# Kernel optimization log

Measured on AMD Instinct MI355X. Metric: run time of the kernel, lower is better.

## Reference

```python
import jax, jax.numpy as jnp
import numpy as np

B, N, DIM = 16, 1024, 768
H, HD = 12, 64  # num_heads, head_dim


def rotate_half(x):
    x1, x2 = jnp.split(x, 2, axis=-1)
    return jnp.concatenate((-x2, x1), axis=-1)


def setup_inputs() -> dict:
    key = jax.random.key(0)
    k1, k2, k3, k4, k5 = jax.random.split(key, 5)
    x = jax.random.normal(k1, (B, N, DIM), dtype=jnp.float32)
    # precomputed 2D-RoPE angles for the 32x32 patch grid: (N, head_dim)
    sin = jax.random.uniform(k2, (N, HD), dtype=jnp.float32, minval=-1.0, maxval=1.0)
    cos = jax.random.uniform(k3, (N, HD), dtype=jnp.float32, minval=-1.0, maxval=1.0)
    # params: qkv (no bias), proj (with bias)
    W_qkv = jax.random.normal(k4, (DIM, 3 * H * HD), dtype=jnp.float32) / np.sqrt(DIM)
    W_proj = jax.random.normal(k5, (H * HD, DIM), dtype=jnp.float32) / np.sqrt(H * HD)
    b_proj = jnp.zeros((DIM,), dtype=jnp.float32)
    return {"x": x, "sin": sin, "cos": cos, "W_qkv": W_qkv, "W_proj": W_proj, "b_proj": b_proj}


def reference(x, sin, cos, W_qkv, W_proj, b_proj):
    b, n, _ = x.shape
    qkv = (x @ W_qkv).reshape(b, n, 3, H, HD)
    q, k, v = jnp.moveaxis(qkv, 2, 0)          # each (b, n, H, HD)
    q = jnp.swapaxes(q, 1, 2)                  # (b, H, n, HD)
    k = jnp.swapaxes(k, 1, 2)
    v = jnp.swapaxes(v, 1, 2)
    # RoPE (prefix_tokens=0: apply to all tokens); sin/cos broadcast (n,HD)->(1,1,n,HD)
    s = sin[None, None]
    c = cos[None, None]
    q = q * c + rotate_half(q) * s
    k = k * c + rotate_half(k) * s
    # scaled dot-product attention (non-causal, no mask, no dropout)
    scale = 1.0 / jnp.sqrt(jnp.asarray(HD, dtype=q.dtype))
    scores = jnp.einsum('bhqd,bhkd->bhqk', q, k) * scale
    attn = jax.nn.softmax(scores, axis=-1)
    out = jnp.einsum('bhqk,bhkd->bhqd', attn, v)
    out = jnp.swapaxes(out, 1, 2).reshape(b, n, H * HD)
    return out @ W_proj + b_proj
```

## Files before the change

kernel.cpp:

```cpp
#include <hip/hip_runtime.h>


typedef __attribute__((ext_vector_type(8))) _Float16 fp16x8;
typedef __attribute__((ext_vector_type(4))) _Float16 h4;
typedef __attribute__((ext_vector_type(4))) float f32x4;

#define MFMA16(a, b, c) __builtin_amdgcn_mfma_f32_16x16x32_f16(a, b, c, 0, 0, 0)

__device__ __forceinline__ float fexp2(float x) {
    float r;
    asm volatile("v_exp_f32 %0, %1\n\ts_nop 0" : "=v"(r) : "v"(x));
    return r;
}

__device__ __forceinline__ void gload16(const _Float16* g, _Float16* s) {
    __builtin_amdgcn_global_load_lds(
        (const __attribute__((address_space(1))) unsigned int*)g,
        (__attribute__((address_space(3))) unsigned int*)s, 16, 0, 0);
}

__global__ __launch_bounds__(256) void tofp16_kernel(const float* __restrict__ in,
                                                     _Float16* __restrict__ outp, int n4) {
    int i = blockIdx.x * 256 + threadIdx.x;
    if (i >= n4) return;
    float4 v = ((const float4*)in)[i];
    h4 o;
    o[0] = (_Float16)v.x;
    o[1] = (_Float16)v.y;
    o[2] = (_Float16)v.z;
    o[3] = (_Float16)v.w;
    *(h4*)(outp + (size_t)i * 4) = o;
}

__global__ __launch_bounds__(256) void ttrans_kernel(const float* __restrict__ W,
                                                     _Float16* __restrict__ outp,
                                                     int rows, int cols) {
    __shared__ float tile[32][33];
    const int c0 = blockIdx.x * 32, r0 = blockIdx.y * 32;
    const int t = threadIdx.x;
#pragma unroll
    for (int i = 0; i < 4; ++i) {
        int idx = t + i * 256;
        int r = idx >> 5, c = idx & 31;
        tile[r][c] = W[(size_t)(r0 + r) * cols + c0 + c];
    }
    __syncthreads();
#pragma unroll
    for (int i = 0; i < 4; ++i) {
        int idx = t + i * 256;
        int rp = idx >> 5, cp = idx & 31;
        outp[(size_t)(c0 + rp) * rows + r0 + cp] = (_Float16)tile[cp][rp];
    }
}

__device__ __forceinline__ void gemm_core8(
    const _Float16* __restrict__ Ag, const _Float16* __restrict__ Bg,
    _Float16* lds, int m0, int n0, f32x4 (&acc)[4][4]) {
    constexpr int BUF = 12288;
    constexpr int OB = 8192;
    const int t = threadIdx.x, l = t & 63, w = t >> 6;
    const int wr = w >> 1, wc = w & 1;
    const int hi = l >> 4, qL = l & 15;

    const int scol = ((t & 3) ^ ((t >> 3) & 3)) << 3;
    const int srow = t >> 2;

    int afo[4], bfo[4];
#pragma unroll
    for (int i = 0; i < 4; ++i) {
        int r = wr * 64 + i * 16 + qL;
        afo[i] = r * 32 + ((hi ^ ((r >> 1) & 3)) << 3);
        int c = wc * 64 + i * 16 + qL;
        bfo[i] = OB + c * 32 + ((hi ^ ((c >> 1) & 3)) << 3);
    }

    auto stageA = [&](int kt, int b) {
        _Float16* base = lds + b * BUF;
        const int k0 = kt * 32;
        gload16(Ag + (size_t)(m0 + srow) * 768 + k0 + scol,
                base + (w * 16) * 32);
        gload16(Ag + (size_t)(m0 + 128 + srow) * 768 + k0 + scol,
                base + (128 + w * 16) * 32);
    };
    auto stageB = [&](int kt, int b) {
        _Float16* base = lds + b * BUF;
        const int k0 = kt * 32;
        gload16(Bg + (size_t)(n0 + srow) * 768 + k0 + scol,
                base + OB + (w * 16) * 32);
    };

    stageA(0, 0);
    stageB(0, 0);
    stageA(1, 1);
    stageB(1, 1);
    asm volatile("s_waitcnt vmcnt(3)" ::: "memory");
    __builtin_amdgcn_s_barrier();

    for (int kt = 0; kt < 24; ++kt) {
        const int bn = (kt + 2) % 3;
        _Float16* bb = lds + (kt % 3) * BUF;

        if (kt < 22) stageA(kt + 2, bn);
        fp16x8 af[4], bf[4];
#pragma unroll
        for (int j = 0; j < 4; ++j) bf[j] = *(const fp16x8*)(bb + bfo[j]);
#pragma unroll
        for (int i = 0; i < 2; ++i) af[i] = *(const fp16x8*)(bb + afo[i]);
        __builtin_amdgcn_s_barrier();
        asm volatile("s_waitcnt lgkmcnt(0)" ::: "memory");
        __builtin_amdgcn_s_setprio(1);
#pragma unroll
        for (int i = 0; i < 2; ++i)
#pragma unroll
            for (int j = 0; j < 4; ++j) acc[i][j] = MFMA16(af[i], bf[j], acc[i][j]);
        __builtin_amdgcn_s_setprio(0);
        __builtin_amdgcn_s_barrier();

        if (kt < 22) stageB(kt + 2, bn);
#pragma unroll
        for (int i = 2; i < 4; ++i) af[i] = *(const fp16x8*)(bb + afo[i]);
        __builtin_amdgcn_s_barrier();
        asm volatile("s_waitcnt lgkmcnt(0)" ::: "memory");
        __builtin_amdgcn_s_setprio(1);
#pragma unroll
        for (int i = 2; i < 4; ++i)
#pragma unroll
            for (int j = 0; j < 4; ++j) acc[i][j] = MFMA16(af[i], bf[j], acc[i][j]);
        __builtin_amdgcn_s_setprio(0);

        if (kt < 22)
            asm volatile("s_waitcnt vmcnt(3)" ::: "memory");
        else
            asm volatile("s_waitcnt vmcnt(0)" ::: "memory");
        __builtin_amdgcn_s_barrier();
    }
}

__global__ __launch_bounds__(512, 4) void qkv_gemm(
    const _Float16* __restrict__ Ag, const _Float16* __restrict__ Bg,
    const float* __restrict__ sinp, const float* __restrict__ cosp,
    _Float16* __restrict__ Qf, _Float16* __restrict__ Kf,
    _Float16* __restrict__ Vt) {
    __shared__ _Float16 lds[3 * 12288];
    const int t = threadIdx.x, l = t & 63, w = t >> 6;
    const int wr = w >> 1, wc = w & 1;
    const int hi = l >> 4, qL = l & 15;

    const int bid = blockIdx.x;
    const int xcd = bid & 7, local = bid >> 3;
    const int m0 = (xcd * 8 + (local & 7)) * 256;
    const int n0 = (local >> 3) * 128;

    f32x4 acc[4][4];
#pragma unroll
    for (int i = 0; i < 4; ++i)
#pragma unroll
        for (int j = 0; j < 4; ++j) acc[i][j] = (f32x4){0.f, 0.f, 0.f, 0.f};

    gemm_core8(Ag, Bg, lds, m0, n0, acc);

    const int colbase = n0 + wc * 64;
    const int sector = colbase / 768;
    const int h = (colbase % 768) >> 6;
    const float SC = 0.18033688011f;

    if (sector == 2) {
#pragma unroll
        for (int ms = 0; ms < 4; ++ms) {
            int mbase = m0 + wr * 64 + ms * 16 + hi * 4;
            int b = mbase >> 10, nb = mbase & 1023;
            int bh = b * 12 + h;
#pragma unroll
            for (int ns = 0; ns < 4; ++ns) {
                int d = ns * 16 + qL;
                h4 pk;
#pragma unroll
                for (int reg = 0; reg < 4; ++reg) pk[reg] = (_Float16)acc[ms][ns][reg];
                *(h4*)(Vt + ((size_t)bh * 64 + d) * 1024 + nb) = pk;
            }
        }
    } else if (sector == 0) {
#pragma unroll
        for (int ms = 0; ms < 4; ++ms) {
#pragma unroll
            for (int reg = 0; reg < 4; ++reg) {
                int m = m0 + wr * 64 + ms * 16 + hi * 4 + reg;
                int b = m >> 10, n = m & 1023;
                size_t base = ((size_t)(b * 12 + h) * 1024 + n) * 64;
#pragma unroll
                for (int p = 0; p < 2; ++p) {
                    int d = p * 16 + qL;
                    float c1 = cosp[n * 64 + d], s1 = sinp[n * 64 + d];
                    float c2 = cosp[n * 64 + d + 32], s2 = sinp[n * 64 + d + 32];
                    float vlo = acc[ms][p][reg], vhi = acc[ms][p + 2][reg];
                    Qf[base + d] = (_Float16)((vlo * c1 - vhi * s1) * SC);
                    Qf[base + d + 32] = (_Float16)((vhi * c2 + vlo * s2) * SC);
                }
            }
        }
    } else {
#pragma unroll
        for (int ms = 0; ms < 4; ++ms) {
#pragma unroll
            for (int reg = 0; reg < 4; ++reg) {
                int m = m0 + wr * 64 + ms * 16 + hi * 4 + reg;
                int b = m >> 10, n = m & 1023;
                size_t base = ((size_t)(b * 12 + h) * 1024 + n) * 64;
#pragma unroll
                for (int p = 0; p < 2; ++p) {
                    int d = p * 16 + qL;
                    float c1 = cosp[n * 64 + d], s1 = sinp[n * 64 + d];
                    float c2 = cosp[n * 64 + d + 32], s2 = sinp[n * 64 + d + 32];
                    float vlo = acc[ms][p][reg], vhi = acc[ms][p + 2][reg];
                    Kf[base + d] = (_Float16)(vlo * c1 - vhi * s1);
                    Kf[base + d + 32] = (_Float16)(vhi * c2 + vlo * s2);
                }
            }
        }
    }
}

__global__ __launch_bounds__(512, 4) void proj_gemm(
    const _Float16* __restrict__ Ag, const _Float16* __restrict__ Bg,
    const float* __restrict__ bias, float* __restrict__ out) {
    __shared__ _Float16 lds[3 * 12288];
    const int t = threadIdx.x, l = t & 63, w = t >> 6;
    const int wr = w >> 1, wc = w & 1;
    const int hi = l >> 4, qL = l & 15;

    const int bid = blockIdx.x;
    const int xcd = bid & 7, local = bid >> 3;
    const int m0 = (xcd * 8 + (local & 7)) * 256;
    const int n0 = (local >> 3) * 128;

    f32x4 acc[4][4];
#pragma unroll
    for (int i = 0; i < 4; ++i)
#pragma unroll
        for (int j = 0; j < 4; ++j) acc[i][j] = (f32x4){0.f, 0.f, 0.f, 0.f};

    gemm_core8(Ag, Bg, lds, m0, n0, acc);

#pragma unroll
    for (int ms = 0; ms < 4; ++ms) {
#pragma unroll
        for (int ns = 0; ns < 4; ++ns) {
            int col = n0 + wc * 64 + ns * 16 + qL;
            float bv = bias[col];
#pragma unroll
            for (int reg = 0; reg < 4; ++reg) {
                int m = m0 + wr * 64 + ms * 16 + hi * 4 + reg;
                out[(size_t)m * 768 + col] = acc[ms][ns][reg] + bv;
            }
        }
    }
}

__global__ __launch_bounds__(256, 3) void attn_kernel(
    const _Float16* __restrict__ Qf, const _Float16* __restrict__ Kfg,
    const _Float16* __restrict__ Vtg, _Float16* __restrict__ aof) {
    __shared__ _Float16 khs[2][64][64];
    __shared__ _Float16 vts[2][64][64];
    __shared__ _Float16 pbuf[4][32][72];

    const int t = threadIdx.x, l = t & 63, w = t >> 6;
    const int flat = blockIdx.x;
    const int xcd = flat & 7, idx = flat >> 3;
    const int bh = xcd * 24 + (idx >> 3);
    const int n0 = (idx & 7) * 128;
    const int bq = bh / 12, hh = bh % 12;
    const size_t base = (size_t)bh << 16;
    const int hi = l >> 4, qL = l & 15;

    fp16x8 qf[2][2];
#pragma unroll
    for (int q2 = 0; q2 < 2; ++q2)
#pragma unroll
        for (int kk = 0; kk < 2; ++kk) {
            size_t off = base + (size_t)(n0 + w * 32 + q2 * 16 + qL) * 64 +
                         kk * 32 + (hi << 3);
            qf[q2][kk] = *(const fp16x8*)(Qf + off);
        }

    const int r0 = w * 16;
    const int srow = l >> 3;
    const int scol = ((l & 7) ^ srow) << 3;
    const _Float16* kf_src = Kfg + base + (size_t)(r0 + srow) * 64 + scol;
    const _Float16* vt_src = Vtg + base + (size_t)(r0 + srow) * 1024 + scol;

    int kfo[4][2];
#pragma unroll
    for (int c = 0; c < 4; ++c)
#pragma unroll
        for (int kk = 0; kk < 2; ++kk) {
            int row = c * 16 + qL;
            int col16 = (kk << 2) | hi;
            kfo[c][kk] = row * 64 + ((col16 ^ (row & 7)) << 3);
        }

    f32x4 ot[4][2];
    float l_part[2] = {0.f, 0.f};
#pragma unroll
    for (int q2 = 0; q2 < 2; ++q2)
#pragma unroll
        for (int dt = 0; dt < 4; ++dt) ot[dt][q2] = (f32x4){0.f, 0.f, 0.f, 0.f};

    auto stage = [&](int kt, int b) {
        const _Float16* ks = kf_src + (size_t)kt * 4096;
        gload16(ks, &khs[b][r0][0]);
        gload16(ks + 512, &khs[b][r0 + 8][0]);
        const _Float16* vs = vt_src + kt * 64;
        gload16(vs, &vts[b][r0][0]);
        gload16(vs + 8 * 1024, &vts[b][r0 + 8][0]);
    };

    stage(0, 0);
    __syncthreads();

    for (int kt = 0; kt < 16; ++kt) {
        const int cur = kt & 1;
        if (kt < 15) stage(kt + 1, cur ^ 1);

        const _Float16* kb = &khs[cur][0][0];
        const _Float16* vb = &vts[cur][0][0];

        f32x4 s[4][2];
#pragma unroll
        for (int c = 0; c < 4; ++c) {
            fp16x8 kf0 = *(const fp16x8*)(kb + kfo[c][0]);
            fp16x8 kf1 = *(const fp16x8*)(kb + kfo[c][1]);
#pragma unroll
            for (int q2 = 0; q2 < 2; ++q2) {
                f32x4 a = (f32x4){0.f, 0.f, 0.f, 0.f};
                a = MFMA16(kf0, qf[q2][0], a);
                a = MFMA16(kf1, qf[q2][1], a);
                s[c][q2] = a;
            }
        }

#pragma unroll
        for (int q2 = 0; q2 < 2; ++q2) {
            const int prow = q2 * 16 + qL;
            float lsum = 0.f;
#pragma unroll
            for (int c = 0; c < 4; ++c) {
                float p0 = fexp2(s[c][q2][0] - 4.0f);
                float p1 = fexp2(s[c][q2][1] - 4.0f);
                float p2 = fexp2(s[c][q2][2] - 4.0f);
                float p3 = fexp2(s[c][q2][3] - 4.0f);
                lsum += (p0 + p1) + (p2 + p3);
                h4 pk;
                pk[0] = (_Float16)p0;
                pk[1] = (_Float16)p1;
                pk[2] = (_Float16)p2;
                pk[3] = (_Float16)p3;
                *(h4*)&pbuf[w][prow][c * 16 + (hi << 2)] = pk;
            }
            l_part[q2] += lsum;
        }

        fp16x8 pf[2][2];
#pragma unroll
        for (int q2 = 0; q2 < 2; ++q2)
#pragma unroll
            for (int ss = 0; ss < 2; ++ss)
                pf[q2][ss] = *(const fp16x8*)&pbuf[w][q2 * 16 + qL][ss * 32 + (hi << 3)];

#pragma unroll
        for (int dt = 0; dt < 4; ++dt) {
            fp16x8 v0 = *(const fp16x8*)(vb + kfo[dt][0]);
            fp16x8 v1 = *(const fp16x8*)(vb + kfo[dt][1]);
#pragma unroll
            for (int q2 = 0; q2 < 2; ++q2) {
                ot[dt][q2] = MFMA16(v0, pf[q2][0], ot[dt][q2]);
                ot[dt][q2] = MFMA16(v1, pf[q2][1], ot[dt][q2]);
            }
        }

        __syncthreads();
    }

#pragma unroll
    for (int q2 = 0; q2 < 2; ++q2) {
        float ls = l_part[q2];
        ls += __shfl_xor(ls, 16);
        ls += __shfl_xor(ls, 32);
        float inv = 1.0f / ls;
        int n = n0 + w * 32 + q2 * 16 + qL;
        size_t rowoff = ((size_t)(bq * 1024 + n)) * 768 + hh * 64 + (hi << 2);
#pragma unroll
        for (int dt = 0; dt < 4; ++dt) {
            h4 r;
#pragma unroll
            for (int reg = 0; reg < 4; ++reg) r[reg] = (_Float16)(ot[dt][q2][reg] * inv);
            *(h4*)(aof + rowoff + dt * 16) = r;
        }
    }
}

extern "C" void kernel_launch(void* const* d_in, const int* in_sizes, int n_in,
                              void* d_out, int out_size, void* d_ws, size_t ws_size,
                              hipStream_t stream) {
    const float* x = (const float*)d_in[0];
    const float* sinp = (const float*)d_in[1];
    const float* cosp = (const float*)d_in[2];
    const float* Wqkv = (const float*)d_in[3];
    const float* Wproj = (const float*)d_in[4];
    const float* bproj = (const float*)d_in[5];
    float* out = (float*)d_out;

    char* ws = (char*)d_ws;
    _Float16* xf  = (_Float16*)(ws);
    _Float16* wqt = (_Float16*)(ws + 25165824);
    _Float16* wpt = (_Float16*)(ws + 28704768);
    _Float16* Qf  = (_Float16*)(ws + 29884416);
    _Float16* Kf  = (_Float16*)(ws + 55050240);
    _Float16* Vt  = (_Float16*)(ws + 80216064);
    _Float16* aof = xf;

    tofp16_kernel<<<12288, 256, 0, stream>>>(x, xf, 3145728);
    ttrans_kernel<<<dim3(72, 24), 256, 0, stream>>>(Wqkv, wqt, 768, 2304);
    ttrans_kernel<<<dim3(24, 24), 256, 0, stream>>>(Wproj, wpt, 768, 768);
    qkv_gemm<<<1152, 512, 0, stream>>>(xf, wqt, sinp, cosp, Qf, Kf, Vt);
    attn_kernel<<<1536, 256, 0, stream>>>(Qf, Kf, Vt, aof);
    proj_gemm<<<384, 512, 0, stream>>>(aof, wpt, bproj, out);
}
```

Measured before the change: 194.7 us.

## Shrink GEMM tiles to 128x128 with 256-thread blocks and precompute interleaved RoPE table

Both GEMMs change from 256x128 tiles with 512 threads to 128x128 tiles with 256 threads. This doubles the grid size and cuts LDS use per block, and the staging loads and vmcnt waits are adjusted to match. A small new kernel packs cos/sin pairs into a float4 table, so the RoPE epilogue does one vector load where it used to do four scalar loads. The cost is lower per-block data reuse: A is now reloaded for every N tile with more blocks. It also adds one extra kernel launch.

```diff
diff --git a/kernel.cpp b/kernel.cpp
--- a/kernel.cpp
+++ b/kernel.cpp
@@ -53,11 +53,24 @@
     }
 }
 
-__device__ __forceinline__ void gemm_core8(
+__global__ __launch_bounds__(256) void ropetab_kernel(const float* __restrict__ sinp,
+                                                      const float* __restrict__ cosp,
+                                                      float4* __restrict__ tab) {
+    int idx = blockIdx.x * 256 + threadIdx.x;
+    int n = idx >> 5, d = idx & 31;
+    float4 v;
+    v.x = cosp[n * 64 + d];
+    v.y = sinp[n * 64 + d];
+    v.z = cosp[n * 64 + d + 32];
+    v.w = sinp[n * 64 + d + 32];
+    tab[idx] = v;
+}
+
+__device__ __forceinline__ void gemm_core128(
     const _Float16* __restrict__ Ag, const _Float16* __restrict__ Bg,
     _Float16* lds, int m0, int n0, f32x4 (&acc)[4][4]) {
-    constexpr int BUF = 12288;
-    constexpr int OB = 8192;
+    constexpr int BUF = 8192;
+    constexpr int OB = 4096;
     const int t = threadIdx.x, l = t & 63, w = t >> 6;
     const int wr = w >> 1, wc = w & 1;
     const int hi = l >> 4, qL = l & 15;
@@ -77,23 +90,24 @@
     auto stageA = [&](int kt, int b) {
         _Float16* base = lds + b * BUF;
         const int k0 = kt * 32;
-        gload16(Ag + (size_t)(m0 + srow) * 768 + k0 + scol,
-                base + (w * 16) * 32);
-        gload16(Ag + (size_t)(m0 + 128 + srow) * 768 + k0 + scol,
-                base + (128 + w * 16) * 32);
+        gload16(Ag + (size_t)(m0 + srow) * 768 + k0 + scol, base + (w * 16) * 32);
+        gload16(Ag + (size_t)(m0 + 64 + srow) * 768 + k0 + scol,
+                base + (64 + w * 16) * 32);
     };
     auto stageB = [&](int kt, int b) {
         _Float16* base = lds + b * BUF;
         const int k0 = kt * 32;
         gload16(Bg + (size_t)(n0 + srow) * 768 + k0 + scol,
                 base + OB + (w * 16) * 32);
+        gload16(Bg + (size_t)(n0 + 64 + srow) * 768 + k0 + scol,
+                base + OB + (64 + w * 16) * 32);
     };
 
     stageA(0, 0);
     stageB(0, 0);
     stageA(1, 1);
     stageB(1, 1);
-    asm volatile("s_waitcnt vmcnt(3)" ::: "memory");
+    asm volatile("s_waitcnt vmcnt(4)" ::: "memory");
     __builtin_amdgcn_s_barrier();
 
     for (int kt = 0; kt < 24; ++kt) {
@@ -129,27 +143,26 @@
         __builtin_amdgcn_s_setprio(0);
 
         if (kt < 22)
-            asm volatile("s_waitcnt vmcnt(3)" ::: "memory");
+            asm volatile("s_waitcnt vmcnt(4)" ::: "memory");
         else
             asm volatile("s_waitcnt vmcnt(0)" ::: "memory");
         __builtin_amdgcn_s_barrier();
     }
 }
 
-__global__ __launch_bounds__(512, 4) void qkv_gemm(
+__global__ __launch_bounds__(256, 3) void qkv_gemm(
     const _Float16* __restrict__ Ag, const _Float16* __restrict__ Bg,
-    const float* __restrict__ sinp, const float* __restrict__ cosp,
-    _Float16* __restrict__ Qf, _Float16* __restrict__ Kf,
-    _Float16* __restrict__ Vt) {
-    __shared__ _Float16 lds[3 * 12288];
+    const float4* __restrict__ tab, _Float16* __restrict__ Qf,
+    _Float16* __restrict__ Kf, _Float16* __restrict__ Vt) {
+    __shared__ _Float16 lds[3 * 8192];
     const int t = threadIdx.x, l = t & 63, w = t >> 6;
     const int wr = w >> 1, wc = w & 1;
     const int hi = l >> 4, qL = l & 15;
 
     const int bid = blockIdx.x;
     const int xcd = bid & 7, local = bid >> 3;
-    const int m0 = (xcd * 8 + (local & 7)) * 256;
-    const int n0 = (local >> 3) * 128;
+    const int m0 = (xcd * 16 + (local & 15)) * 128;
+    const int n0 = (local >> 4) * 128;
 
     f32x4 acc[4][4];
 #pragma unroll
@@ -157,7 +170,7 @@
 #pragma unroll
         for (int j = 0; j < 4; ++j) acc[i][j] = (f32x4){0.f, 0.f, 0.f, 0.f};
 
-    gemm_core8(Ag, Bg, lds, m0, n0, acc);
+    gemm_core128(Ag, Bg, lds, m0, n0, acc);
 
     const int colbase = n0 + wc * 64;
     const int sector = colbase / 768;
@@ -190,11 +203,10 @@
 #pragma unroll
                 for (int p = 0; p < 2; ++p) {
                     int d = p * 16 + qL;
-                    float c1 = cosp[n * 64 + d], s1 = sinp[n * 64 + d];
-                    float c2 = cosp[n * 64 + d + 32], s2 = sinp[n * 64 + d + 32];
+                    float4 cs = tab[n * 32 + d];
                     float vlo = acc[ms][p][reg], vhi = acc[ms][p + 2][reg];
-                    Qf[base + d] = (_Float16)((vlo * c1 - vhi * s1) * SC);
-                    Qf[base + d + 32] = (_Float16)((vhi * c2 + vlo * s2) * SC);
+                    Qf[base + d] = (_Float16)((vlo * cs.x - vhi * cs.y) * SC);
+                    Qf[base + d + 32] = (_Float16)((vhi * cs.z + vlo * cs.w) * SC);
                 }
             }
         }
@@ -209,29 +221,28 @@
 #pragma unroll
                 for (int p = 0; p < 2; ++p) {
                     int d = p * 16 + qL;
-                    float c1 = cosp[n * 64 + d], s1 = sinp[n * 64 + d];
-                    float c2 = cosp[n * 64 + d + 32], s2 = sinp[n * 64 + d + 32];
+                    float4 cs = tab[n * 32 + d];
                     float vlo = acc[ms][p][reg], vhi = acc[ms][p + 2][reg];
-                    Kf[base + d] = (_Float16)(vlo * c1 - vhi * s1);
-                    Kf[base + d + 32] = (_Float16)(vhi * c2 + vlo * s2);
+                    Kf[base + d] = (_Float16)(vlo * cs.x - vhi * cs.y);
+                    Kf[base + d + 32] = (_Float16)(vhi * cs.z + vlo * cs.w);
                 }
             }
         }
     }
 }
 
-__global__ __launch_bounds__(512, 4) void proj_gemm(
+__global__ __launch_bounds__(256, 3) void proj_gemm(
     const _Float16* __restrict__ Ag, const _Float16* __restrict__ Bg,
     const float* __restrict__ bias, float* __restrict__ out) {
-    __shared__ _Float16 lds[3 * 12288];
+    __shared__ _Float16 lds[3 * 8192];
     const int t = threadIdx.x, l = t & 63, w = t >> 6;
     const int wr = w >> 1, wc = w & 1;
     const int hi = l >> 4, qL = l & 15;
 
     const int bid = blockIdx.x;
     const int xcd = bid & 7, local = bid >> 3;
-    const int m0 = (xcd * 8 + (local & 7)) * 256;
-    const int n0 = (local >> 3) * 128;
+    const int m0 = (xcd * 16 + (local & 15)) * 128;
+    const int n0 = (local >> 4) * 128;
 
     f32x4 acc[4][4];
 #pragma unroll
@@ -239,7 +250,7 @@
 #pragma unroll
         for (int j = 0; j < 4; ++j) acc[i][j] = (f32x4){0.f, 0.f, 0.f, 0.f};
 
-    gemm_core8(Ag, Bg, lds, m0, n0, acc);
+    gemm_core128(Ag, Bg, lds, m0, n0, acc);
 
 #pragma unroll
     for (int ms = 0; ms < 4; ++ms) {
@@ -416,12 +427,14 @@
     _Float16* Qf  = (_Float16*)(ws + 29884416);
     _Float16* Kf  = (_Float16*)(ws + 55050240);
     _Float16* Vt  = (_Float16*)(ws + 80216064);
+    float4*   tab = (float4*)(ws + 105381888);
     _Float16* aof = xf;
 
     tofp16_kernel<<<12288, 256, 0, stream>>>(x, xf, 3145728);
     ttrans_kernel<<<dim3(72, 24), 256, 0, stream>>>(Wqkv, wqt, 768, 2304);
     ttrans_kernel<<<dim3(24, 24), 256, 0, stream>>>(Wproj, wpt, 768, 768);
-    qkv_gemm<<<1152, 512, 0, stream>>>(xf, wqt, sinp, cosp, Qf, Kf, Vt);
+    ropetab_kernel<<<128, 256, 0, stream>>>(sinp, cosp, tab);
+    qkv_gemm<<<2304, 256, 0, stream>>>(xf, wqt, tab, Qf, Kf, Vt);
     attn_kernel<<<1536, 256, 0, stream>>>(Qf, Kf, Vt, aof);
-    proj_gemm<<<384, 512, 0, stream>>>(aof, wpt, bproj, out);
-}
+    proj_gemm<<<768, 256, 0, stream>>>(aof, wpt, bproj, out);
+}
```

After: 200.4 us. 3.0% more time.

## Swap MFMA operands for row-contiguous epilogue stores and split QKV GEMM

Applied to the files above, without the earlier changes.

For the Q/K and projection GEMMs, the MFMA operands are swapped so each lane's accumulator holds 4 consecutive columns of a single row. This lets the epilogues write packed h4 or float4 vectors instead of scattered scalar stores. A small kernel interleaves cos/sin into a float4 table so the RoPE epilogue loads one float4 per element instead of four scalars. The fused QKV GEMM is split into a Q/K launch and a separate V launch so each keeps its own store layout, at the cost of two extra kernel launches and a tail boundary between the GEMMs.

```diff
diff --git a/kernel.cpp b/kernel.cpp
--- a/kernel.cpp
+++ b/kernel.cpp
@@ -53,6 +53,20 @@
     }
 }
 
+__global__ __launch_bounds__(256) void ropetab_kernel(const float* __restrict__ sinp,
+                                                      const float* __restrict__ cosp,
+                                                      float4* __restrict__ tab) {
+    int idx = blockIdx.x * 256 + threadIdx.x;
+    int n = idx >> 5, d = idx & 31;
+    float4 v;
+    v.x = cosp[n * 64 + d];
+    v.y = sinp[n * 64 + d];
+    v.z = cosp[n * 64 + d + 32];
+    v.w = sinp[n * 64 + d + 32];
+    tab[idx] = v;
+}
+
+template <bool SWAP>
 __device__ __forceinline__ void gemm_core8(
     const _Float16* __restrict__ Ag, const _Float16* __restrict__ Bg,
     _Float16* lds, int m0, int n0, f32x4 (&acc)[4][4]) {
@@ -112,7 +126,12 @@
 #pragma unroll
         for (int i = 0; i < 2; ++i)
 #pragma unroll
-            for (int j = 0; j < 4; ++j) acc[i][j] = MFMA16(af[i], bf[j], acc[i][j]);
+            for (int j = 0; j < 4; ++j) {
+                if constexpr (SWAP)
+                    acc[i][j] = MFMA16(bf[j], af[i], acc[i][j]);
+                else
+                    acc[i][j] = MFMA16(af[i], bf[j], acc[i][j]);
+            }
         __builtin_amdgcn_s_setprio(0);
         __builtin_amdgcn_s_barrier();
 
@@ -125,7 +144,12 @@
 #pragma unroll
         for (int i = 2; i < 4; ++i)
 #pragma unroll
-            for (int j = 0; j < 4; ++j) acc[i][j] = MFMA16(af[i], bf[j], acc[i][j]);
+            for (int j = 0; j < 4; ++j) {
+                if constexpr (SWAP)
+                    acc[i][j] = MFMA16(bf[j], af[i], acc[i][j]);
+                else
+                    acc[i][j] = MFMA16(af[i], bf[j], acc[i][j]);
+            }
         __builtin_amdgcn_s_setprio(0);
 
         if (kt < 22)
@@ -136,10 +160,59 @@
     }
 }
 
-__global__ __launch_bounds__(512, 4) void qkv_gemm(
+__global__ __launch_bounds__(512, 4) void qkv_qk_gemm(
     const _Float16* __restrict__ Ag, const _Float16* __restrict__ Bg,
-    const float* __restrict__ sinp, const float* __restrict__ cosp,
-    _Float16* __restrict__ Qf, _Float16* __restrict__ Kf,
+    const float4* __restrict__ tab, _Float16* __restrict__ Qf,
+    _Float16* __restrict__ Kf) {
+    __shared__ _Float16 lds[3 * 12288];
+    const int t = threadIdx.x, l = t & 63, w = t >> 6;
+    const int wr = w >> 1, wc = w & 1;
+    const int hi = l >> 4, qL = l & 15;
+
+    const int bid = blockIdx.x;
+    const int xcd = bid & 7, local = bid >> 3;
+    const int m0 = (xcd * 8 + (local & 7)) * 256;
+    const int n0 = (local >> 3) * 128;
+
+    f32x4 acc[4][4];
+#pragma unroll
+    for (int i = 0; i < 4; ++i)
+#pragma unroll
+        for (int j = 0; j < 4; ++j) acc[i][j] = (f32x4){0.f, 0.f, 0.f, 0.f};
+
+    gemm_core8<true>(Ag, Bg, lds, m0, n0, acc);
+
+    const int colbase = n0 + wc * 64;
+    const int sector = colbase / 768;
+    const int h = (colbase % 768) >> 6;
+    _Float16* dst = (sector == 0) ? Qf : Kf;
+    const float SC = (sector == 0) ? 0.18033688011f : 1.0f;
+
+#pragma unroll
+    for (int ms = 0; ms < 4; ++ms) {
+        int m = m0 + wr * 64 + ms * 16 + qL;
+        int b = m >> 10, n = m & 1023;
+        size_t base = ((size_t)(b * 12 + h) * 1024 + n) * 64;
+#pragma unroll
+        for (int ns = 0; ns < 2; ++ns) {
+            int d0 = ns * 16 + hi * 4;
+            h4 lo4, hi4;
+#pragma unroll
+            for (int reg = 0; reg < 4; ++reg) {
+                int d = d0 + reg;
+                float4 cs = tab[n * 32 + d];
+                float vlo = acc[ms][ns][reg], vhi = acc[ms][ns + 2][reg];
+                lo4[reg] = (_Float16)((vlo * cs.x - vhi * cs.y) * SC);
+                hi4[reg] = (_Float16)((vhi * cs.z + vlo * cs.w) * SC);
+            }
+            *(h4*)(dst + base + d0) = lo4;
+            *(h4*)(dst + base + d0 + 32) = hi4;
+        }
+    }
+}
+
+__global__ __launch_bounds__(512, 4) void qkv_v_gemm(
+    const _Float16* __restrict__ Ag, const _Float16* __restrict__ Bg,
     _Float16* __restrict__ Vt) {
     __shared__ _Float16 lds[3 * 12288];
     const int t = threadIdx.x, l = t & 63, w = t >> 6;
@@ -149,7 +222,7 @@
     const int bid = blockIdx.x;
     const int xcd = bid & 7, local = bid >> 3;
     const int m0 = (xcd * 8 + (local & 7)) * 256;
-    const int n0 = (local >> 3) * 128;
+    const int n0 = (12 + (local >> 3)) * 128;
 
     f32x4 acc[4][4];
 #pragma unroll
@@ -157,65 +230,22 @@
 #pragma unroll
         for (int j = 0; j < 4; ++j) acc[i][j] = (f32x4){0.f, 0.f, 0.f, 0.f};
 
-    gemm_core8(Ag, Bg, lds, m0, n0, acc);
-
-    const int colbase = n0 + wc * 64;
-    const int sector = colbase / 768;
-    const int h = (colbase % 768) >> 6;
-    const float SC = 0.18033688011f;
-
-    if (sector == 2) {
-#pragma unroll
-        for (int ms = 0; ms < 4; ++ms) {
-            int mbase = m0 + wr * 64 + ms * 16 + hi * 4;
-            int b = mbase >> 10, nb = mbase & 1023;
-            int bh = b * 12 + h;
-#pragma unroll
-            for (int ns = 0; ns < 4; ++ns) {
-                int d = ns * 16 + qL;
-                h4 pk;
-#pragma unroll
-                for (int reg = 0; reg < 4; ++reg) pk[reg] = (_Float16)acc[ms][ns][reg];
-                *(h4*)(Vt + ((size_t)bh * 64 + d) * 1024 + nb) = pk;
-            }
-        }
-    } else if (sector == 0) {
-#pragma unroll
-        for (int ms = 0; ms < 4; ++ms) {
-#pragma unroll
-            for (int reg = 0; reg < 4; ++reg) {
-                int m = m0 + wr * 64 + ms * 16 + hi * 4 + reg;
-                int b = m >> 10, n = m & 1023;
-                size_t base = ((size_t)(b * 12 + h) * 1024 + n) * 64;
-#pragma unroll
-                for (int p = 0; p < 2; ++p) {
-                    int d = p * 16 + qL;
-                    float c1 = cosp[n * 64 + d], s1 = sinp[n * 64 + d];
-                    float c2 = cosp[n * 64 + d + 32], s2 = sinp[n * 64 + d + 32];
-                    float vlo = acc[ms][p][reg], vhi = acc[ms][p + 2][reg];
-                    Qf[base + d] = (_Float16)((vlo * c1 - vhi * s1) * SC);
-                    Qf[base + d + 32] = (_Float16)((vhi * c2 + vlo * s2) * SC);
-                }
-            }
-        }
-    } else {
-#pragma unroll
-        for (int ms = 0; ms < 4; ++ms) {
-#pragma unroll
-            for (int reg = 0; reg < 4; ++reg) {
-                int m = m0 + wr * 64 + ms * 16 + hi * 4 + reg;
-                int b = m >> 10, n = m & 1023;
-                size_t base = ((size_t)(b * 12 + h) * 1024 + n) * 64;
-#pragma unroll
-                for (int p = 0; p < 2; ++p) {
-                    int d = p * 16 + qL;
-                    float c1 = cosp[n * 64 + d], s1 = sinp[n * 64 + d];
-                    float c2 = cosp[n * 64 + d + 32], s2 = sinp[n * 64 + d + 32];
-                    float vlo = acc[ms][p][reg], vhi = acc[ms][p + 2][reg];
-                    Kf[base + d] = (_Float16)(vlo * c1 - vhi * s1);
-                    Kf[base + d + 32] = (_Float16)(vhi * c2 + vlo * s2);
-                }
-            }
+    gemm_core8<false>(Ag, Bg, lds, m0, n0, acc);
+
+    const int h = ((n0 + wc * 64) % 768) >> 6;
+
+#pragma unroll
+    for (int ms = 0; ms < 4; ++ms) {
+        int mbase = m0 + wr * 64 + ms * 16 + hi * 4;
+        int b = mbase >> 10, nb = mbase & 1023;
+        int bh = b * 12 + h;
+#pragma unroll
+        for (int ns = 0; ns < 4; ++ns) {
+            int d = ns * 16 + qL;
+            h4 pk;
+#pragma unroll
+            for (int reg = 0; reg < 4; ++reg) pk[reg] = (_Float16)acc[ms][ns][reg];
+            *(h4*)(Vt + ((size_t)bh * 64 + d) * 1024 + nb) = pk;
         }
     }
 }
@@ -239,19 +269,21 @@
 #pragma unroll
         for (int j = 0; j < 4; ++j) acc[i][j] = (f32x4){0.f, 0.f, 0.f, 0.f};
 
-    gemm_core8(Ag, Bg, lds, m0, n0, acc);
+    gemm_core8<true>(Ag, Bg, lds, m0, n0, acc);
 
 #pragma unroll
     for (int ms = 0; ms < 4; ++ms) {
+        int m = m0 + wr * 64 + ms * 16 + qL;
 #pragma unroll
         for (int ns = 0; ns < 4; ++ns) {
-            int col = n0 + wc * 64 + ns * 16 + qL;
-            float bv = bias[col];
-#pragma unroll
-            for (int reg = 0; reg < 4; ++reg) {
-                int m = m0 + wr * 64 + ms * 16 + hi * 4 + reg;
-                out[(size_t)m * 768 + col] = acc[ms][ns][reg] + bv;
-            }
+            int c = n0 + wc * 64 + ns * 16 + hi * 4;
+            float4 bv = *(const float4*)(bias + c);
+            float4 r;
+            r.x = acc[ms][ns][0] + bv.x;
+            r.y = acc[ms][ns][1] + bv.y;
+            r.z = acc[ms][ns][2] + bv.z;
+            r.w = acc[ms][ns][3] + bv.w;
+            *(float4*)(out + (size_t)m * 768 + c) = r;
         }
     }
 }
@@ -416,12 +448,15 @@
     _Float16* Qf  = (_Float16*)(ws + 29884416);
     _Float16* Kf  = (_Float16*)(ws + 55050240);
     _Float16* Vt  = (_Float16*)(ws + 80216064);
+    float4*   tab = (float4*)(ws + 105381888);
     _Float16* aof = xf;
 
     tofp16_kernel<<<12288, 256, 0, stream>>>(x, xf, 3145728);
     ttrans_kernel<<<dim3(72, 24), 256, 0, stream>>>(Wqkv, wqt, 768, 2304);
     ttrans_kernel<<<dim3(24, 24), 256, 0, stream>>>(Wproj, wpt, 768, 768);
-    qkv_gemm<<<1152, 512, 0, stream>>>(xf, wqt, sinp, cosp, Qf, Kf, Vt);
+    ropetab_kernel<<<128, 256, 0, stream>>>(sinp, cosp, tab);
+    qkv_qk_gemm<<<768, 512, 0, stream>>>(xf, wqt, tab, Qf, Kf);
+    qkv_v_gemm<<<384, 512, 0, stream>>>(xf, wqt, Vt);
     attn_kernel<<<1536, 256, 0, stream>>>(Qf, Kf, Vt, aof);
     proj_gemm<<<384, 512, 0, stream>>>(aof, wpt, bproj, out);
 }
```

New measurement: 217.3 us. 11.6% more time.

## Stage QKV epilogue through LDS for coalesced 16-byte stores and pack RoPE table

Applied to the files above, without the earlier changes.

The QKV GEMM epilogue now writes rotated Q/K and transposed V tiles into shared memory first, then emits coalesced 16-byte vector stores to global memory instead of scattered 2-byte and 8-byte stores. A small new kernel interleaves cos/sin into a float4 table so each epilogue element needs one vector load rather than four scalar loads. This adds a barrier, LDS traffic and an extra tiny launch, and reuses the GEMM's LDS buffer after the main loop.

```diff
diff --git a/kernel.cpp b/kernel.cpp
--- a/kernel.cpp
+++ b/kernel.cpp
@@ -51,6 +51,19 @@
         int rp = idx >> 5, cp = idx & 31;
         outp[(size_t)(c0 + rp) * rows + r0 + cp] = (_Float16)tile[cp][rp];
     }
+}
+
+__global__ __launch_bounds__(256) void ropetab_kernel(const float* __restrict__ sinp,
+                                                      const float* __restrict__ cosp,
+                                                      float4* __restrict__ tab) {
+    int idx = blockIdx.x * 256 + threadIdx.x;
+    int n = idx >> 5, d = idx & 31;
+    float4 v;
+    v.x = cosp[n * 64 + d];
+    v.y = sinp[n * 64 + d];
+    v.z = cosp[n * 64 + d + 32];
+    v.w = sinp[n * 64 + d + 32];
+    tab[idx] = v;
 }
 
 __device__ __forceinline__ void gemm_core8(
@@ -138,9 +151,8 @@
 
 __global__ __launch_bounds__(512, 4) void qkv_gemm(
     const _Float16* __restrict__ Ag, const _Float16* __restrict__ Bg,
-    const float* __restrict__ sinp, const float* __restrict__ cosp,
-    _Float16* __restrict__ Qf, _Float16* __restrict__ Kf,
-    _Float16* __restrict__ Vt) {
+    const float4* __restrict__ tab, _Float16* __restrict__ Qf,
+    _Float16* __restrict__ Kf, _Float16* __restrict__ Vt) {
     __shared__ _Float16 lds[3 * 12288];
     const int t = threadIdx.x, l = t & 63, w = t >> 6;
     const int wr = w >> 1, wc = w & 1;
@@ -159,63 +171,64 @@
 
     gemm_core8(Ag, Bg, lds, m0, n0, acc);
 
-    const int colbase = n0 + wc * 64;
-    const int sector = colbase / 768;
-    const int h = (colbase % 768) >> 6;
-    const float SC = 0.18033688011f;
+    const int sector = n0 / 768;
+    const int hbase = (n0 % 768) >> 6;
 
     if (sector == 2) {
 #pragma unroll
         for (int ms = 0; ms < 4; ++ms) {
-            int mbase = m0 + wr * 64 + ms * 16 + hi * 4;
-            int b = mbase >> 10, nb = mbase & 1023;
-            int bh = b * 12 + h;
+            int mlb = wr * 64 + ms * 16 + hi * 4;
 #pragma unroll
             for (int ns = 0; ns < 4; ++ns) {
-                int d = ns * 16 + qL;
+                int col = wc * 64 + ns * 16 + qL;
                 h4 pk;
 #pragma unroll
                 for (int reg = 0; reg < 4; ++reg) pk[reg] = (_Float16)acc[ms][ns][reg];
-                *(h4*)(Vt + ((size_t)bh * 64 + d) * 1024 + nb) = pk;
-            }
-        }
-    } else if (sector == 0) {
+                *(h4*)&lds[col * 264 + mlb] = pk;
+            }
+        }
+        __syncthreads();
+        const int b = m0 >> 10, nst = m0 & 1023;
+#pragma unroll
+        for (int it = 0; it < 8; ++it) {
+            int task = it * 512 + t;
+            int j = task & 31, col = task >> 5;
+            fp16x8 v = *(const fp16x8*)&lds[col * 264 + j * 8];
+            int h = hbase + (col >> 6), d = col & 63;
+            *(fp16x8*)(Vt + ((size_t)(b * 12 + h) * 64 + d) * 1024 + nst + j * 8) = v;
+        }
+    } else {
+        const float SC = (sector == 0) ? 0.18033688011f : 1.0f;
 #pragma unroll
         for (int ms = 0; ms < 4; ++ms) {
 #pragma unroll
             for (int reg = 0; reg < 4; ++reg) {
-                int m = m0 + wr * 64 + ms * 16 + hi * 4 + reg;
-                int b = m >> 10, n = m & 1023;
-                size_t base = ((size_t)(b * 12 + h) * 1024 + n) * 64;
+                int ml = wr * 64 + ms * 16 + hi * 4 + reg;
+                int n = (m0 + ml) & 1023;
 #pragma unroll
                 for (int p = 0; p < 2; ++p) {
                     int d = p * 16 + qL;
-                    float c1 = cosp[n * 64 + d], s1 = sinp[n * 64 + d];
-                    float c2 = cosp[n * 64 + d + 32], s2 = sinp[n * 64 + d + 32];
+                    float4 cs = tab[n * 32 + d];
                     float vlo = acc[ms][p][reg], vhi = acc[ms][p + 2][reg];
-                    Qf[base + d] = (_Float16)((vlo * c1 - vhi * s1) * SC);
-                    Qf[base + d + 32] = (_Float16)((vhi * c2 + vlo * s2) * SC);
+                    lds[ml * 136 + wc * 64 + d] =
+                        (_Float16)((vlo * cs.x - vhi * cs.y) * SC);
+                    lds[ml * 136 + wc * 64 + d + 32] =
+                        (_Float16)((vhi * cs.z + vlo * cs.w) * SC);
                 }
             }
         }
-    } else {
-#pragma unroll
-        for (int ms = 0; ms < 4; ++ms) {
-#pragma unroll
-            for (int reg = 0; reg < 4; ++reg) {
-                int m = m0 + wr * 64 + ms * 16 + hi * 4 + reg;
-                int b = m >> 10, n = m & 1023;
-                size_t base = ((size_t)(b * 12 + h) * 1024 + n) * 64;
-#pragma unroll
-                for (int p = 0; p < 2; ++p) {
-                    int d = p * 16 + qL;
-                    float c1 = cosp[n * 64 + d], s1 = sinp[n * 64 + d];
-                    float c2 = cosp[n * 64 + d + 32], s2 = sinp[n * 64 + d + 32];
-                    float vlo = acc[ms][p][reg], vhi = acc[ms][p + 2][reg];
-                    Kf[base + d] = (_Float16)(vlo * c1 - vhi * s1);
-                    Kf[base + d + 32] = (_Float16)(vhi * c2 + vlo * s2);
-                }
-            }
+        __syncthreads();
+        _Float16* dst = (sector == 0) ? Qf : Kf;
+#pragma unroll
+        for (int it = 0; it < 8; ++it) {
+            int task = it * 512 + t;
+            int j = task & 7;
+            int r = (task >> 3) & 255;
+            int hf = task >> 11;
+            fp16x8 v = *(const fp16x8*)&lds[r * 136 + hf * 64 + j * 8];
+            int b = (m0 + r) >> 10, n = (m0 + r) & 1023;
+            int h = hbase + hf;
+            *(fp16x8*)(dst + ((size_t)(b * 12 + h) * 1024 + n) * 64 + j * 8) = v;
         }
     }
 }
@@ -416,12 +429,14 @@
     _Float16* Qf  = (_Float16*)(ws + 29884416);
     _Float16* Kf  = (_Float16*)(ws + 55050240);
     _Float16* Vt  = (_Float16*)(ws + 80216064);
+    float4*   tab = (float4*)(ws + 105381888);
     _Float16* aof = xf;
 
     tofp16_kernel<<<12288, 256, 0, stream>>>(x, xf, 3145728);
     ttrans_kernel<<<dim3(72, 24), 256, 0, stream>>>(Wqkv, wqt, 768, 2304);
     ttrans_kernel<<<dim3(24, 24), 256, 0, stream>>>(Wproj, wpt, 768, 768);
-    qkv_gemm<<<1152, 512, 0, stream>>>(xf, wqt, sinp, cosp, Qf, Kf, Vt);
+    ropetab_kernel<<<128, 256, 0, stream>>>(sinp, cosp, tab);
+    qkv_gemm<<<1152, 512, 0, stream>>>(xf, wqt, tab, Qf, Kf, Vt);
     attn_kernel<<<1536, 256, 0, stream>>>(Qf, Kf, Vt, aof);
     proj_gemm<<<384, 512, 0, stream>>>(aof, wpt, bproj, out);
 }
```

New measurement: 189.9 us. 2.4% less time.
